# Kernel tuning notes

Hardware: AMD Instinct MI355X
Metric: run time of the kernel (lower is better)

Reference implementation:

```python
import jax, jax.numpy as jnp
import numpy as np


def setup_inputs() -> dict:
    key = jax.random.key(0)
    k1, k2 = jax.random.split(key)
    B, H, N, D = 4, 16, 2048, 64
    x = jax.random.normal(k1, (B, H, N, D), dtype=jnp.float32)
    wqkv = 0.02 * jax.random.normal(k2, (H, D, 3 * D), dtype=jnp.float32)
    bqkv = jnp.zeros((H, 1, 3 * D), dtype=jnp.float32)
    return {"x": x, "wqkv": wqkv, "bqkv": bqkv}


def reference(x, wqkv, bqkv):
    # x: [B, H, N, D]; wqkv: [H, D, 3D]; bqkv: [H, 1, 3D]
    B, H, N, D = x.shape
    scale = D ** (-0.5)
    qkv = jnp.einsum('bhnd,hde->bhne', x, wqkv) + bqkv  # [B,H,N,3D]
    # Faithful to torch: reshape (3D,) -> (D, 3) then unbind last axis,
    # i.e. q/k/v are interleaved (stride-3) columns of the projection.
    qkv = qkv.reshape(B, H, N, D, 3)
    q = qkv[..., 0] * scale
    k = qkv[..., 1]
    v = qkv[..., 2]
    attn = jnp.einsum('bhqd,bhkd->bhqk', q, k)  # [B,H,N,N]
    attn = jax.nn.softmax(attn, axis=-1)
    out = jnp.einsum('bhqk,bhkd->bhqd', attn, v)  # [B,H,N,D]
    return out
```

## Files before the change

### kernel.cpp

```cpp
#include <hip/hip_runtime.h>
#include <hip/hip_bf16.h>
#include <stdint.h>

typedef short bf16x8 __attribute__((ext_vector_type(8)));
typedef short bf16x4 __attribute__((ext_vector_type(4)));
typedef float f32x4 __attribute__((ext_vector_type(4)));

#define BHC 64
#define NQ 2048
#define DD 64
#define NE 192
#define LDP 72
#define WPS (64 * LDP + 8)
#define PLP 36
#define QSCALE 0.1803368801111245f

__device__ __forceinline__ short f2bf(float f) {
  unsigned u = __float_as_uint(f);
  unsigned r = (u + 0x7FFFu + ((u >> 16) & 1u)) >> 16;
  return (short)r;
}

__device__ __forceinline__ bf16x8 pack8(float4 a, float4 b) {
  bf16x8 v;
  v[0] = f2bf(a.x); v[1] = f2bf(a.y); v[2] = f2bf(a.z); v[3] = f2bf(a.w);
  v[4] = f2bf(b.x); v[5] = f2bf(b.y); v[6] = f2bf(b.z); v[7] = f2bf(b.w);
  return v;
}

__device__ __forceinline__ short2 pk_bf16(float a, float b) {
  __hip_bfloat162 c = __float22bfloat162_rn(make_float2(a, b));
  return *reinterpret_cast<short2*>(&c);
}

__global__ __launch_bounds__(256, 4) void proj_kernel(
    const float* __restrict__ x, const float* __restrict__ w,
    const float* __restrict__ bq, short* __restrict__ Qg,
    short* __restrict__ Kg, short* __restrict__ Vtg) {
  __shared__ short wt[3 * WPS];
  __shared__ short sV[4][64 * 24];

  const int tid = threadIdx.x;
  const int bh = blockIdx.x >> 5;
  const int rb = blockIdx.x & 31;
  const int h = bh & 15;

  const float* whp = w + (size_t)h * DD * NE;
  for (int i = 0; i < 48; ++i) {
    int idx = i * 256 + tid;
    int d = idx / NE, e = idx - d * NE;
    int dd = e / 3, wh = e - dd * 3;
    wt[wh * WPS + dd * LDP + d] = f2bf(whp[idx]);
  }
  __syncthreads();

  const int wave = tid >> 6;
  const int lane = tid & 63;
  const int col = lane & 15, quad = lane >> 4;
  const int row0 = rb * 64 + wave * 16;

  const float* xrow = x + ((size_t)bh * NQ + row0 + col) * DD;
  bf16x8 aq[2];
#pragma unroll
  for (int kc = 0; kc < 2; ++kc) {
    const float4* p4 = (const float4*)(xrow + kc * 32 + quad * 8);
    aq[kc] = pack8(p4[0], p4[1]);
  }

  f32x4 acc[12];
#pragma unroll
  for (int nt = 0; nt < 12; ++nt) acc[nt] = (f32x4){0.f, 0.f, 0.f, 0.f};

#pragma unroll
  for (int nt = 0; nt < 12; ++nt) {
    const short* wrow = &wt[(nt >> 2) * WPS + ((nt & 3) * 16 + col) * LDP];
#pragma unroll
    for (int kc = 0; kc < 2; ++kc) {
      bf16x8 bw = *(const bf16x8*)(wrow + kc * 32 + quad * 8);
      acc[nt] = __builtin_amdgcn_mfma_f32_16x16x32_bf16(aq[kc], bw, acc[nt], 0, 0, 0);
    }
  }

  const float* bqh = bq + h * NE;
  short* Qp = Qg + ((size_t)bh * NQ + row0) * DD;
  short* Kp = Kg + ((size_t)bh * NQ + row0) * DD;
  short* sVw = sV[wave];

#pragma unroll
  for (int nt = 0; nt < 12; ++nt) {
    int dd = (nt & 3) * 16 + col;
    float bias = bqh[dd * 3 + (nt >> 2)];
    float v0 = acc[nt][0] + bias, v1 = acc[nt][1] + bias;
    float v2 = acc[nt][2] + bias, v3 = acc[nt][3] + bias;
    if (nt < 4) { v0 *= QSCALE; v1 *= QSCALE; v2 *= QSCALE; v3 *= QSCALE; }
    short2 s01 = pk_bf16(v0, v1);
    short2 s23 = pk_bf16(v2, v3);
    int rowl = quad * 4;
    if (nt < 4) {
      Qp[rowl * DD + dd] = s01.x; Qp[(rowl + 1) * DD + dd] = s01.y;
      Qp[(rowl + 2) * DD + dd] = s23.x; Qp[(rowl + 3) * DD + dd] = s23.y;
    } else if (nt < 8) {
      Kp[rowl * DD + dd] = s01.x; Kp[(rowl + 1) * DD + dd] = s01.y;
      Kp[(rowl + 2) * DD + dd] = s23.x; Kp[(rowl + 3) * DD + dd] = s23.y;
    } else {
      sVw[dd * 24 + rowl] = s01.x; sVw[dd * 24 + rowl + 1] = s01.y;
      sVw[dd * 24 + rowl + 2] = s23.x; sVw[dd * 24 + rowl + 3] = s23.y;
    }
  }

  short* Vp = Vtg + (size_t)bh * DD * NQ + row0;
#pragma unroll
  for (int c = 0; c < 2; ++c) {
    int idx = c * 64 + lane;
    int d = idx >> 1, half = (idx & 1) * 8;
    *(bf16x8*)(Vp + (size_t)d * NQ + half) = *(const bf16x8*)(sVw + d * 24 + half);
  }
}

__global__ __launch_bounds__(256, 2) void attn_kernel(
    const short* __restrict__ Qg, const short* __restrict__ Kg,
    const short* __restrict__ Vtg, float* __restrict__ out) {
  __shared__ short kbuf[2][64 * 64];
  __shared__ short vbuf[2][64 * 64];
  __shared__ short pbuf[4][64 * PLP];

  const int tid = threadIdx.x;
  const int bh = blockIdx.x & 63;
  const int qb = blockIdx.x >> 6;
  const int wave = tid >> 6, lane = tid & 63;
  const int col = lane & 15, quad = lane >> 4;
  const int qbase = qb * 256 + wave * 64;

  bf16x8 bqf[4][2];
#pragma unroll
  for (int ntq = 0; ntq < 4; ++ntq)
#pragma unroll
    for (int kc = 0; kc < 2; ++kc)
      bqf[ntq][kc] = *(const bf16x8*)(Qg + ((size_t)bh * NQ + qbase + ntq * 16 + col) * DD +
                                      kc * 32 + quad * 8);

  bf16x8 onesf;
#pragma unroll
  for (int j = 0; j < 8; ++j) onesf[j] = (short)0x3F80;

  f32x4 o[4][4];
  f32x4 l4[4];
#pragma unroll
  for (int mtq = 0; mtq < 4; ++mtq) {
    l4[mtq] = (f32x4){0.f, 0.f, 0.f, 0.f};
#pragma unroll
    for (int ntd = 0; ntd < 4; ++ntd) o[mtq][ntd] = (f32x4){0.f, 0.f, 0.f, 0.f};
  }

  short* pb = pbuf[wave];
  const short* Kb = Kg + (size_t)bh * NQ * DD;
  const short* Vb = Vtg + (size_t)bh * DD * NQ;

  const int r0 = tid >> 3, c0 = tid & 7;
  const int dst0 = r0 * 64 + ((c0 ^ (r0 & 7)) * 8);
  const int dst1 = (r0 + 32) * 64 + ((c0 ^ (r0 & 7)) * 8);
  const int src0 = r0 * DD + c0 * 8;
  const size_t vsrc0o = (size_t)r0 * NQ + c0 * 8;
  const size_t vsrc1o = (size_t)(r0 + 32) * NQ + c0 * 8;

  {
    bf16x8 k0 = *(const bf16x8*)(Kb + src0);
    bf16x8 k1 = *(const bf16x8*)(Kb + src0 + 32 * DD);
    bf16x8 v0 = *(const bf16x8*)(Vb + vsrc0o);
    bf16x8 v1 = *(const bf16x8*)(Vb + vsrc1o);
    *(bf16x8*)(&kbuf[0][dst0]) = k0;
    *(bf16x8*)(&kbuf[0][dst1]) = k1;
    *(bf16x8*)(&vbuf[0][dst0]) = v0;
    *(bf16x8*)(&vbuf[0][dst1]) = v1;
  }
  __syncthreads();

#pragma unroll 1
  for (int t = 0; t < 32; ++t) {
    const int p = t & 1;
    const short* kb = kbuf[p];
    const short* vb_s = vbuf[p];

    bf16x8 nk0, nk1, nv0, nv1;
    if (t < 31) {
      const short* Kn = Kb + (t + 1) * 64 * DD;
      const short* Vn = Vb + (t + 1) * 64;
      nk0 = *(const bf16x8*)(Kn + src0);
      nk1 = *(const bf16x8*)(Kn + src0 + 32 * DD);
      nv0 = *(const bf16x8*)(Vn + vsrc0o);
      nv1 = *(const bf16x8*)(Vn + vsrc1o);
    }

#pragma unroll
    for (int h = 0; h < 2; ++h) {
#pragma unroll
      for (int j = 0; j < 2; ++j) {
        const int krow = (2 * h + j) * 16 + col;
        const int kx = krow & 7;
        bf16x8 ka0 = *(const bf16x8*)(&kb[krow * 64 + ((quad ^ kx) * 8)]);
        bf16x8 ka1 = *(const bf16x8*)(&kb[krow * 64 + (((4 + quad) ^ kx) * 8)]);
#pragma unroll
        for (int ntq = 0; ntq < 4; ++ntq) {
          f32x4 s = (f32x4){0.f, 0.f, 0.f, 0.f};
          s = __builtin_amdgcn_mfma_f32_16x16x32_bf16(ka0, bqf[ntq][0], s, 0, 0, 0);
          s = __builtin_amdgcn_mfma_f32_16x16x32_bf16(ka1, bqf[ntq][1], s, 0, 0, 0);
          float p0 = __builtin_amdgcn_exp2f(s[0]);
          float p1 = __builtin_amdgcn_exp2f(s[1]);
          float p2 = __builtin_amdgcn_exp2f(s[2]);
          float p3 = __builtin_amdgcn_exp2f(s[3]);
          short2 s01 = pk_bf16(p0, p1);
          short2 s23 = pk_bf16(p2, p3);
          bf16x4 pv; pv[0] = s01.x; pv[1] = s01.y; pv[2] = s23.x; pv[3] = s23.y;
          *(bf16x4*)(&pb[(ntq * 16 + col) * PLP + j * 16 + quad * 4]) = pv;
        }
      }

#pragma unroll
      for (int mtq = 0; mtq < 4; ++mtq) {
        bf16x8 ap = *(const bf16x8*)(&pb[(mtq * 16 + col) * PLP + quad * 8]);
#pragma unroll
        for (int ntd = 0; ntd < 4; ++ntd) {
          const int vrow = ntd * 16 + col;
          bf16x8 vf = *(const bf16x8*)(&vb_s[vrow * 64 + (((h * 4 + quad) ^ (vrow & 7)) * 8)]);
          o[mtq][ntd] = __builtin_amdgcn_mfma_f32_16x16x32_bf16(ap, vf, o[mtq][ntd], 0, 0, 0);
        }
        l4[mtq] = __builtin_amdgcn_mfma_f32_16x16x32_bf16(ap, onesf, l4[mtq], 0, 0, 0);
      }
    }

    if (t < 31) {
      short* kn = kbuf[1 - p];
      short* vn = vbuf[1 - p];
      *(bf16x8*)(&kn[dst0]) = nk0;
      *(bf16x8*)(&kn[dst1]) = nk1;
      *(bf16x8*)(&vn[dst0]) = nv0;
      *(bf16x8*)(&vn[dst1]) = nv1;
      __syncthreads();
    }
  }

#pragma unroll
  for (int mtq = 0; mtq < 4; ++mtq) {
#pragma unroll
    for (int r = 0; r < 4; ++r) {
      float inv = 1.0f / l4[mtq][r];
      int rq = qbase + mtq * 16 + quad * 4 + r;
      float* orow = out + ((size_t)bh * NQ + rq) * DD;
#pragma unroll
      for (int ntd = 0; ntd < 4; ++ntd) orow[ntd * 16 + col] = o[mtq][ntd][r] * inv;
    }
  }
}

extern "C" void kernel_launch(void* const* d_in, const int* in_sizes, int n_in,
                              void* d_out, int out_size, void* d_ws, size_t ws_size,
                              hipStream_t stream) {
  const float* x = (const float*)d_in[0];
  const float* w = (const float*)d_in[1];
  const float* bq = (const float*)d_in[2];
  float* out = (float*)d_out;

  short* Qg = (short*)d_ws;
  short* Kg = Qg + (size_t)BHC * NQ * DD;
  short* Vtg = Kg + (size_t)BHC * NQ * DD;

  proj_kernel<<<dim3(2048), dim3(256), 0, stream>>>(x, w, bq, Qg, Kg, Vtg);
  attn_kernel<<<dim3(512), dim3(256), 0, stream>>>(Qg, Kg, Vtg, out);
}
```

Before: 203.4 us.

## Load K/V fragments straight from global into registers and restructure both kernels

The attention kernel drops its LDS double-buffered K/V staging and barriers. Each wave now loads its K and V MFMA fragments directly from global memory into a register double buffer, using 128-thread blocks and twice as many blocks. The row-sum is computed with scalar adds plus cross-lane shuffles instead of an extra MFMA against a ones vector. The projection kernel now handles four row tiles per block with x prefetch, which amortises the weight transpose into LDS. The trade-off is that each wave re-reads K/V from global/L2 with no sharing across waves, and register pressure goes up.

```diff
diff --git a/kernel.cpp b/kernel.cpp
--- a/kernel.cpp
+++ b/kernel.cpp
@@ -12,7 +12,6 @@
 #define NE 192
 #define LDP 72
 #define WPS (64 * LDP + 8)
-#define PLP 36
 #define QSCALE 0.1803368801111245f
 
 __device__ __forceinline__ short f2bf(float f) {
@@ -33,7 +32,7 @@
   return *reinterpret_cast<short2*>(&c);
 }
 
-__global__ __launch_bounds__(256, 4) void proj_kernel(
+__global__ __launch_bounds__(256, 2) void proj_kernel(
     const float* __restrict__ x, const float* __restrict__ w,
     const float* __restrict__ bq, short* __restrict__ Qg,
     short* __restrict__ Kg, short* __restrict__ Vtg) {
@@ -41,8 +40,8 @@
   __shared__ short sV[4][64 * 24];
 
   const int tid = threadIdx.x;
-  const int bh = blockIdx.x >> 5;
-  const int rb = blockIdx.x & 31;
+  const int bh = blockIdx.x >> 3;
+  const int g = blockIdx.x & 7;
   const int h = bh & 15;
 
   const float* whp = w + (size_t)h * DD * NE;
@@ -57,79 +56,87 @@
   const int wave = tid >> 6;
   const int lane = tid & 63;
   const int col = lane & 15, quad = lane >> 4;
-  const int row0 = rb * 64 + wave * 16;
-
-  const float* xrow = x + ((size_t)bh * NQ + row0 + col) * DD;
-  bf16x8 aq[2];
-#pragma unroll
-  for (int kc = 0; kc < 2; ++kc) {
-    const float4* p4 = (const float4*)(xrow + kc * 32 + quad * 8);
-    aq[kc] = pack8(p4[0], p4[1]);
-  }
-
-  f32x4 acc[12];
-#pragma unroll
-  for (int nt = 0; nt < 12; ++nt) acc[nt] = (f32x4){0.f, 0.f, 0.f, 0.f};
-
-#pragma unroll
-  for (int nt = 0; nt < 12; ++nt) {
-    const short* wrow = &wt[(nt >> 2) * WPS + ((nt & 3) * 16 + col) * LDP];
+  const float* bqh = bq + h * NE;
+  short* sVw = sV[wave];
+
+  auto load_x = [&](int i, bf16x8 dst[2]) {
+    int row0 = (g * 4 + i) * 64 + wave * 16;
+    const float* xrow = x + ((size_t)bh * NQ + row0 + col) * DD;
 #pragma unroll
     for (int kc = 0; kc < 2; ++kc) {
-      bf16x8 bw = *(const bf16x8*)(wrow + kc * 32 + quad * 8);
-      acc[nt] = __builtin_amdgcn_mfma_f32_16x16x32_bf16(aq[kc], bw, acc[nt], 0, 0, 0);
-    }
-  }
-
-  const float* bqh = bq + h * NE;
-  short* Qp = Qg + ((size_t)bh * NQ + row0) * DD;
-  short* Kp = Kg + ((size_t)bh * NQ + row0) * DD;
-  short* sVw = sV[wave];
-
-#pragma unroll
-  for (int nt = 0; nt < 12; ++nt) {
-    int dd = (nt & 3) * 16 + col;
-    float bias = bqh[dd * 3 + (nt >> 2)];
-    float v0 = acc[nt][0] + bias, v1 = acc[nt][1] + bias;
-    float v2 = acc[nt][2] + bias, v3 = acc[nt][3] + bias;
-    if (nt < 4) { v0 *= QSCALE; v1 *= QSCALE; v2 *= QSCALE; v3 *= QSCALE; }
-    short2 s01 = pk_bf16(v0, v1);
-    short2 s23 = pk_bf16(v2, v3);
-    int rowl = quad * 4;
-    if (nt < 4) {
-      Qp[rowl * DD + dd] = s01.x; Qp[(rowl + 1) * DD + dd] = s01.y;
-      Qp[(rowl + 2) * DD + dd] = s23.x; Qp[(rowl + 3) * DD + dd] = s23.y;
-    } else if (nt < 8) {
-      Kp[rowl * DD + dd] = s01.x; Kp[(rowl + 1) * DD + dd] = s01.y;
-      Kp[(rowl + 2) * DD + dd] = s23.x; Kp[(rowl + 3) * DD + dd] = s23.y;
-    } else {
-      sVw[dd * 24 + rowl] = s01.x; sVw[dd * 24 + rowl + 1] = s01.y;
-      sVw[dd * 24 + rowl + 2] = s23.x; sVw[dd * 24 + rowl + 3] = s23.y;
-    }
-  }
-
-  short* Vp = Vtg + (size_t)bh * DD * NQ + row0;
-#pragma unroll
-  for (int c = 0; c < 2; ++c) {
-    int idx = c * 64 + lane;
-    int d = idx >> 1, half = (idx & 1) * 8;
-    *(bf16x8*)(Vp + (size_t)d * NQ + half) = *(const bf16x8*)(sVw + d * 24 + half);
-  }
-}
-
-__global__ __launch_bounds__(256, 2) void attn_kernel(
+      const float4* p4 = (const float4*)(xrow + kc * 32 + quad * 8);
+      dst[kc] = pack8(p4[0], p4[1]);
+    }
+  };
+
+  bf16x8 aq[2][2];
+  load_x(0, aq[0]);
+
+#pragma unroll
+  for (int i = 0; i < 4; ++i) {
+    if (i < 3) load_x(i + 1, aq[(i + 1) & 1]);
+    const bf16x8* a = aq[i & 1];
+    const int row0 = (g * 4 + i) * 64 + wave * 16;
+
+    f32x4 acc[12];
+#pragma unroll
+    for (int nt = 0; nt < 12; ++nt) acc[nt] = (f32x4){0.f, 0.f, 0.f, 0.f};
+
+#pragma unroll
+    for (int nt = 0; nt < 12; ++nt) {
+      const short* wrow = &wt[(nt >> 2) * WPS + ((nt & 3) * 16 + col) * LDP];
+#pragma unroll
+      for (int kc = 0; kc < 2; ++kc) {
+        bf16x8 bw = *(const bf16x8*)(wrow + kc * 32 + quad * 8);
+        acc[nt] = __builtin_amdgcn_mfma_f32_16x16x32_bf16(a[kc], bw, acc[nt], 0, 0, 0);
+      }
+    }
+
+    short* Qp = Qg + ((size_t)bh * NQ + row0) * DD;
+    short* Kp = Kg + ((size_t)bh * NQ + row0) * DD;
+#pragma unroll
+    for (int nt = 0; nt < 12; ++nt) {
+      int dd = (nt & 3) * 16 + col;
+      float bias = bqh[dd * 3 + (nt >> 2)];
+      float v0 = acc[nt][0] + bias, v1 = acc[nt][1] + bias;
+      float v2 = acc[nt][2] + bias, v3 = acc[nt][3] + bias;
+      if (nt < 4) { v0 *= QSCALE; v1 *= QSCALE; v2 *= QSCALE; v3 *= QSCALE; }
+      short2 s01 = pk_bf16(v0, v1);
+      short2 s23 = pk_bf16(v2, v3);
+      int rowl = quad * 4;
+      if (nt < 4) {
+        Qp[rowl * DD + dd] = s01.x; Qp[(rowl + 1) * DD + dd] = s01.y;
+        Qp[(rowl + 2) * DD + dd] = s23.x; Qp[(rowl + 3) * DD + dd] = s23.y;
+      } else if (nt < 8) {
+        Kp[rowl * DD + dd] = s01.x; Kp[(rowl + 1) * DD + dd] = s01.y;
+        Kp[(rowl + 2) * DD + dd] = s23.x; Kp[(rowl + 3) * DD + dd] = s23.y;
+      } else {
+        sVw[dd * 24 + rowl] = s01.x; sVw[dd * 24 + rowl + 1] = s01.y;
+        sVw[dd * 24 + rowl + 2] = s23.x; sVw[dd * 24 + rowl + 3] = s23.y;
+      }
+    }
+
+    short* Vp = Vtg + (size_t)bh * DD * NQ + row0;
+#pragma unroll
+    for (int c = 0; c < 2; ++c) {
+      int idx = c * 64 + lane;
+      int d = idx >> 1, half = (idx & 1) * 8;
+      *(bf16x8*)(Vp + (size_t)d * NQ + half) = *(const bf16x8*)(sVw + d * 24 + half);
+    }
+  }
+}
+
+__global__ __launch_bounds__(128, 2) void attn_kernel(
     const short* __restrict__ Qg, const short* __restrict__ Kg,
     const short* __restrict__ Vtg, float* __restrict__ out) {
-  __shared__ short kbuf[2][64 * 64];
-  __shared__ short vbuf[2][64 * 64];
-  __shared__ short pbuf[4][64 * PLP];
+  __shared__ short pbuf[2][64 * LDP];
 
   const int tid = threadIdx.x;
   const int bh = blockIdx.x & 63;
   const int qb = blockIdx.x >> 6;
   const int wave = tid >> 6, lane = tid & 63;
   const int col = lane & 15, quad = lane >> 4;
-  const int qbase = qb * 256 + wave * 64;
+  const int qbase = qb * 128 + wave * 64;
 
   bf16x8 bqf[4][2];
 #pragma unroll
@@ -139,15 +146,11 @@
       bqf[ntq][kc] = *(const bf16x8*)(Qg + ((size_t)bh * NQ + qbase + ntq * 16 + col) * DD +
                                       kc * 32 + quad * 8);
 
-  bf16x8 onesf;
-#pragma unroll
-  for (int j = 0; j < 8; ++j) onesf[j] = (short)0x3F80;
-
   f32x4 o[4][4];
-  f32x4 l4[4];
+  float l_acc[4];
 #pragma unroll
   for (int mtq = 0; mtq < 4; ++mtq) {
-    l4[mtq] = (f32x4){0.f, 0.f, 0.f, 0.f};
+    l_acc[mtq] = 0.f;
 #pragma unroll
     for (int ntd = 0; ntd < 4; ++ntd) o[mtq][ntd] = (f32x4){0.f, 0.f, 0.f, 0.f};
   }
@@ -156,94 +159,69 @@
   const short* Kb = Kg + (size_t)bh * NQ * DD;
   const short* Vb = Vtg + (size_t)bh * DD * NQ;
 
-  const int r0 = tid >> 3, c0 = tid & 7;
-  const int dst0 = r0 * 64 + ((c0 ^ (r0 & 7)) * 8);
-  const int dst1 = (r0 + 32) * 64 + ((c0 ^ (r0 & 7)) * 8);
-  const int src0 = r0 * DD + c0 * 8;
-  const size_t vsrc0o = (size_t)r0 * NQ + c0 * 8;
-  const size_t vsrc1o = (size_t)(r0 + 32) * NQ + c0 * 8;
-
-  {
-    bf16x8 k0 = *(const bf16x8*)(Kb + src0);
-    bf16x8 k1 = *(const bf16x8*)(Kb + src0 + 32 * DD);
-    bf16x8 v0 = *(const bf16x8*)(Vb + vsrc0o);
-    bf16x8 v1 = *(const bf16x8*)(Vb + vsrc1o);
-    *(bf16x8*)(&kbuf[0][dst0]) = k0;
-    *(bf16x8*)(&kbuf[0][dst1]) = k1;
-    *(bf16x8*)(&vbuf[0][dst0]) = v0;
-    *(bf16x8*)(&vbuf[0][dst1]) = v1;
-  }
-  __syncthreads();
-
+  bf16x8 ka[2][4][2], vf[2][4][2];
+
+  auto load_tile = [&](int t, int buf) {
+    const short* Kt = Kb + t * 64 * DD;
+    const short* Vt = Vb + t * 64;
+#pragma unroll
+    for (int mt = 0; mt < 4; ++mt)
+#pragma unroll
+      for (int kc = 0; kc < 2; ++kc) {
+        ka[buf][mt][kc] = *(const bf16x8*)(Kt + (mt * 16 + col) * DD + kc * 32 + quad * 8);
+        vf[buf][mt][kc] = *(const bf16x8*)(Vt + (size_t)(mt * 16 + col) * NQ + kc * 32 + quad * 8);
+      }
+  };
+
+  auto compute = [&](int t, int buf, bool pf) {
+    if (pf) load_tile(t + 1, buf ^ 1);
+
+#pragma unroll
+    for (int mtk = 0; mtk < 4; ++mtk) {
+#pragma unroll
+      for (int ntq = 0; ntq < 4; ++ntq) {
+        f32x4 s = (f32x4){0.f, 0.f, 0.f, 0.f};
+        s = __builtin_amdgcn_mfma_f32_16x16x32_bf16(ka[buf][mtk][0], bqf[ntq][0], s, 0, 0, 0);
+        s = __builtin_amdgcn_mfma_f32_16x16x32_bf16(ka[buf][mtk][1], bqf[ntq][1], s, 0, 0, 0);
+        float p0 = __builtin_amdgcn_exp2f(s[0]);
+        float p1 = __builtin_amdgcn_exp2f(s[1]);
+        float p2 = __builtin_amdgcn_exp2f(s[2]);
+        float p3 = __builtin_amdgcn_exp2f(s[3]);
+        l_acc[ntq] += (p0 + p1) + (p2 + p3);
+        short2 s01 = pk_bf16(p0, p1);
+        short2 s23 = pk_bf16(p2, p3);
+        bf16x4 pv; pv[0] = s01.x; pv[1] = s01.y; pv[2] = s23.x; pv[3] = s23.y;
+        *(bf16x4*)(&pb[(ntq * 16 + col) * LDP + mtk * 16 + quad * 4]) = pv;
+      }
+    }
+
+#pragma unroll
+    for (int mtq = 0; mtq < 4; ++mtq) {
+      bf16x8 ap0 = *(const bf16x8*)(&pb[(mtq * 16 + col) * LDP + quad * 8]);
+      bf16x8 ap1 = *(const bf16x8*)(&pb[(mtq * 16 + col) * LDP + 32 + quad * 8]);
+#pragma unroll
+      for (int ntd = 0; ntd < 4; ++ntd) {
+        o[mtq][ntd] = __builtin_amdgcn_mfma_f32_16x16x32_bf16(ap0, vf[buf][ntd][0], o[mtq][ntd], 0, 0, 0);
+        o[mtq][ntd] = __builtin_amdgcn_mfma_f32_16x16x32_bf16(ap1, vf[buf][ntd][1], o[mtq][ntd], 0, 0, 0);
+      }
+    }
+  };
+
+  load_tile(0, 0);
 #pragma unroll 1
-  for (int t = 0; t < 32; ++t) {
-    const int p = t & 1;
-    const short* kb = kbuf[p];
-    const short* vb_s = vbuf[p];
-
-    bf16x8 nk0, nk1, nv0, nv1;
-    if (t < 31) {
-      const short* Kn = Kb + (t + 1) * 64 * DD;
-      const short* Vn = Vb + (t + 1) * 64;
-      nk0 = *(const bf16x8*)(Kn + src0);
-      nk1 = *(const bf16x8*)(Kn + src0 + 32 * DD);
-      nv0 = *(const bf16x8*)(Vn + vsrc0o);
-      nv1 = *(const bf16x8*)(Vn + vsrc1o);
-    }
-
-#pragma unroll
-    for (int h = 0; h < 2; ++h) {
-#pragma unroll
-      for (int j = 0; j < 2; ++j) {
-        const int krow = (2 * h + j) * 16 + col;
-        const int kx = krow & 7;
-        bf16x8 ka0 = *(const bf16x8*)(&kb[krow * 64 + ((quad ^ kx) * 8)]);
-        bf16x8 ka1 = *(const bf16x8*)(&kb[krow * 64 + (((4 + quad) ^ kx) * 8)]);
-#pragma unroll
-        for (int ntq = 0; ntq < 4; ++ntq) {
-          f32x4 s = (f32x4){0.f, 0.f, 0.f, 0.f};
-          s = __builtin_amdgcn_mfma_f32_16x16x32_bf16(ka0, bqf[ntq][0], s, 0, 0, 0);
-          s = __builtin_amdgcn_mfma_f32_16x16x32_bf16(ka1, bqf[ntq][1], s, 0, 0, 0);
-          float p0 = __builtin_amdgcn_exp2f(s[0]);
-          float p1 = __builtin_amdgcn_exp2f(s[1]);
-          float p2 = __builtin_amdgcn_exp2f(s[2]);
-          float p3 = __builtin_amdgcn_exp2f(s[3]);
-          short2 s01 = pk_bf16(p0, p1);
-          short2 s23 = pk_bf16(p2, p3);
-          bf16x4 pv; pv[0] = s01.x; pv[1] = s01.y; pv[2] = s23.x; pv[3] = s23.y;
-          *(bf16x4*)(&pb[(ntq * 16 + col) * PLP + j * 16 + quad * 4]) = pv;
-        }
-      }
-
-#pragma unroll
-      for (int mtq = 0; mtq < 4; ++mtq) {
-        bf16x8 ap = *(const bf16x8*)(&pb[(mtq * 16 + col) * PLP + quad * 8]);
-#pragma unroll
-        for (int ntd = 0; ntd < 4; ++ntd) {
-          const int vrow = ntd * 16 + col;
-          bf16x8 vf = *(const bf16x8*)(&vb_s[vrow * 64 + (((h * 4 + quad) ^ (vrow & 7)) * 8)]);
-          o[mtq][ntd] = __builtin_amdgcn_mfma_f32_16x16x32_bf16(ap, vf, o[mtq][ntd], 0, 0, 0);
-        }
-        l4[mtq] = __builtin_amdgcn_mfma_f32_16x16x32_bf16(ap, onesf, l4[mtq], 0, 0, 0);
-      }
-    }
-
-    if (t < 31) {
-      short* kn = kbuf[1 - p];
-      short* vn = vbuf[1 - p];
-      *(bf16x8*)(&kn[dst0]) = nk0;
-      *(bf16x8*)(&kn[dst1]) = nk1;
-      *(bf16x8*)(&vn[dst0]) = nv0;
-      *(bf16x8*)(&vn[dst1]) = nv1;
-      __syncthreads();
-    }
+  for (int tt = 0; tt < 16; ++tt) {
+    compute(2 * tt, 0, true);
+    compute(2 * tt + 1, 1, tt < 15);
   }
 
 #pragma unroll
   for (int mtq = 0; mtq < 4; ++mtq) {
+    float l = l_acc[mtq];
+    l += __shfl_xor(l, 16);
+    l += __shfl_xor(l, 32);
 #pragma unroll
     for (int r = 0; r < 4; ++r) {
-      float inv = 1.0f / l4[mtq][r];
+      float inv = 1.0f / __shfl(l, quad * 4 + r);
       int rq = qbase + mtq * 16 + quad * 4 + r;
       float* orow = out + ((size_t)bh * NQ + rq) * DD;
 #pragma unroll
@@ -264,6 +242,6 @@
   short* Kg = Qg + (size_t)BHC * NQ * DD;
   short* Vtg = Kg + (size_t)BHC * NQ * DD;
 
-  proj_kernel<<<dim3(2048), dim3(256), 0, stream>>>(x, w, bq, Qg, Kg, Vtg);
-  attn_kernel<<<dim3(512), dim3(256), 0, stream>>>(Qg, Kg, Vtg, out);
-}
+  proj_kernel<<<dim3(512), dim3(256), 0, stream>>>(x, w, bq, Qg, Kg, Vtg);
+  attn_kernel<<<dim3(1024), dim3(128), 0, stream>>>(Qg, Kg, Vtg, out);
+}
```

Measured after the change: 303.8 us. 49.3% more time.
